# Kernel optimization log

Hardware: AMD Instinct MI355X
Metric: run time of the kernel (lower is better)

The kernel has to match this reference:

```python
import jax, jax.numpy as jnp
import numpy as np

N, E = 10000, 320000
IN_F, OUT_F = 512, 256
ALPHA = 0.2  # leaky_relu negative slope
NEG_BIG = -9e15


def setup_inputs() -> dict:
    key = jax.random.key(0)
    k1, k2, k3, k4 = jax.random.split(key, 4)
    x = jax.random.normal(k1, (N, IN_F), dtype=jnp.float32)
    # fc: Linear(in_features, out_features) -> W [out, in], b [out] (init to 0 per reset_parameters)
    W = jax.random.normal(k2, (OUT_F, IN_F), dtype=jnp.float32) * (1.414 / np.sqrt(IN_F))
    b = jnp.zeros((OUT_F,), dtype=jnp.float32)
    # att: Conv1d(1,1,2*out) == dot with vector a [2*out]
    a = jax.random.normal(k3, (2 * OUT_F,), dtype=jnp.float32) * (1.414 / np.sqrt(2 * OUT_F))
    edge_list = jax.random.randint(k4, (2, E), 0, N, dtype=jnp.int64)
    return {"x": x, "W": W, "b": b, "a": a, "edge_list": edge_list}


def reference(x, W, b, a, edge_list):
    # eval mode: dropout is identity
    src, tgt = edge_list[0], edge_list[1]
    h = x @ W.T + b  # [N, out]
    out_f = h.shape[1]
    # conv1d over concatenated [h_src, h_tgt] with kernel length 2*out == split dot product
    score = h[src] @ a[:out_f] + h[tgt] @ a[out_f:]  # [E]
    score = jax.nn.leaky_relu(score, negative_slope=ALPHA)
    n = x.shape[0]
    # torch.sparse.FloatTensor(...).to_dense() sums duplicate edges -> scatter-add
    adj = jnp.zeros((n, n), dtype=h.dtype).at[src, tgt].add(score)
    adj = jnp.where(adj == 0, jnp.asarray(NEG_BIG, h.dtype), adj)
    adj = jax.nn.softmax(adj, axis=1)
    return adj @ h  # [N, out]
```

## Files before the change

kernel.cpp:

```cpp
#include <hip/hip_runtime.h>
#include <hip/hip_bf16.h>
#include <math.h>

#define IN_F 512
#define OUT_F 256
#define ALPHA 0.2f
#define CAP 512
#define NCHAIN 16

typedef __attribute__((ext_vector_type(8))) short bf16x8;
typedef __attribute__((ext_vector_type(4))) float f32x4;

static __device__ __forceinline__ unsigned short f2bf(float f) {
  unsigned int u = __builtin_bit_cast(unsigned int, f);
  unsigned int r = (u + 0x7FFFu + ((u >> 16) & 1u)) >> 16;
  return (unsigned short)r;
}

__global__ __launch_bounds__(256) void mega(const float* __restrict__ x,
                                            const float* __restrict__ W,
                                            const float* __restrict__ bias,
                                            const float* __restrict__ a,
                                            const int* __restrict__ edges,
                                            unsigned short* __restrict__ hb,
                                            float* __restrict__ s1p,
                                            float* __restrict__ s2p,
                                            float* __restrict__ hsump,
                                            int* __restrict__ head,
                                            int2* __restrict__ rec,
                                            int N_, int E_, int mtiles, int gblocks) {
  const int tid = threadIdx.x;
  const int vb = blockIdx.x;

  if (vb >= gblocks) {
    int idx = (vb - gblocks) * 256 + tid;
    if (idx < E_) {
      int srcv = edges[idx];
      int tgtv = edges[E_ + idx];
      int old = atomicExch(&head[srcv * NCHAIN + (idx & (NCHAIN - 1))], idx);
      rec[idx] = make_int2(old, tgtv);
    }
    return;
  }

  __shared__ unsigned short lA[64][72];
  __shared__ unsigned short lB[64][72];
  __shared__ float s1t[64], s2t[64], ht[64];

  const int bm = (vb % mtiles) * 64;
  const int bn4 = vb / mtiles;
  const int bn = bn4 * 64;
  const int wave = tid >> 6, lane = tid & 63;
  const int wr = wave >> 1, wc = wave & 1;
  const int lr = lane & 15, lk = lane >> 4;

  f32x4 acc[2][2] = {};

  for (int k0 = 0; k0 < IN_F; k0 += 64) {
#pragma unroll
    for (int r = 0; r < 4; ++r) {
      int idx = tid + r * 256;
      int row = idx >> 4, c4 = idx & 15;
      int gm = bm + row;
      float4 va = (gm < N_) ? *(const float4*)&x[(size_t)gm * IN_F + k0 + c4 * 4]
                            : make_float4(0.f, 0.f, 0.f, 0.f);
      ushort4 oa;
      oa.x = f2bf(va.x); oa.y = f2bf(va.y); oa.z = f2bf(va.z); oa.w = f2bf(va.w);
      *(ushort4*)&lA[row][c4 * 4] = oa;
      float4 vbq = *(const float4*)&W[(size_t)(bn + row) * IN_F + k0 + c4 * 4];
      ushort4 ob;
      ob.x = f2bf(vbq.x); ob.y = f2bf(vbq.y); ob.z = f2bf(vbq.z); ob.w = f2bf(vbq.w);
      *(ushort4*)&lB[row][c4 * 4] = ob;
    }
    __syncthreads();
#pragma unroll
    for (int kk = 0; kk < 64; kk += 32) {
      bf16x8 af[2], bfr[2];
#pragma unroll
      for (int fm = 0; fm < 2; ++fm)
        af[fm] = *(const bf16x8*)&lA[wr * 32 + fm * 16 + lr][kk + lk * 8];
#pragma unroll
      for (int fn = 0; fn < 2; ++fn)
        bfr[fn] = *(const bf16x8*)&lB[wc * 32 + fn * 16 + lr][kk + lk * 8];
#pragma unroll
      for (int fm = 0; fm < 2; ++fm)
#pragma unroll
        for (int fn = 0; fn < 2; ++fn)
          acc[fm][fn] = __builtin_amdgcn_mfma_f32_16x16x32_bf16(af[fm], bfr[fn],
                                                                acc[fm][fn], 0, 0, 0);
    }
    __syncthreads();
  }

  if (tid < 64) { s1t[tid] = 0.f; s2t[tid] = 0.f; ht[tid] = 0.f; }
  __syncthreads();

  int gc[2];
  float av[2], bv[2], biasv[2], csum[2] = {0.f, 0.f};
#pragma unroll
  for (int fn = 0; fn < 2; ++fn) {
    gc[fn] = bn + wc * 32 + fn * 16 + lr;
    av[fn] = a[gc[fn]];
    bv[fn] = a[OUT_F + gc[fn]];
    biasv[fn] = bias[gc[fn]];
  }
#pragma unroll
  for (int fm = 0; fm < 2; ++fm) {
#pragma unroll
    for (int i = 0; i < 4; ++i) {
      int lrow = wr * 32 + fm * 16 + lk * 4 + i;
      int gr = bm + lrow;
      bool valid = (gr < N_);
      float v0 = valid ? acc[fm][0][i] + biasv[0] : 0.f;
      float v1 = valid ? acc[fm][1][i] + biasv[1] : 0.f;
      if (valid) {
        hb[(size_t)gr * OUT_F + gc[0]] = f2bf(v0);
        hb[(size_t)gr * OUT_F + gc[1]] = f2bf(v1);
      }
      csum[0] += v0; csum[1] += v1;
      float p1 = v0 * av[0] + v1 * av[1];
      float p2 = v0 * bv[0] + v1 * bv[1];
#pragma unroll
      for (int off = 1; off < 16; off <<= 1) {
        p1 += __shfl_xor(p1, off);
        p2 += __shfl_xor(p2, off);
      }
      if (lr == 0) {
        atomicAdd(&s1t[lrow], p1);
        atomicAdd(&s2t[lrow], p2);
      }
    }
  }
#pragma unroll
  for (int off = 16; off < 64; off <<= 1) {
    csum[0] += __shfl_xor(csum[0], off);
    csum[1] += __shfl_xor(csum[1], off);
  }
  if (lk == 0) {
    atomicAdd(&ht[wc * 32 + 0 * 16 + lr], csum[0]);
    atomicAdd(&ht[wc * 32 + 1 * 16 + lr], csum[1]);
  }
  __syncthreads();

  if (tid < 64) {
    int gr = bm + tid;
    if (gr < N_) {
      s1p[(size_t)gr * 4 + bn4] = s1t[tid];
      s2p[(size_t)gr * 4 + bn4] = s2t[tid];
    }
    hsump[(size_t)(bm >> 6) * OUT_F + bn + tid] = ht[tid];
  }
}

__global__ __launch_bounds__(256) void rowk(const unsigned short* __restrict__ hb,
                                            const float* __restrict__ s1p,
                                            const float* __restrict__ s2p,
                                            const float* __restrict__ hsump,
                                            int* __restrict__ head,
                                            const int2* __restrict__ rec,
                                            float* __restrict__ out,
                                            int N_, int E_, int mtiles) {
  __shared__ int s_tgt[2][CAP];
  __shared__ float s_w[2][CAP];
  __shared__ int s_len[2][NCHAIN];
  __shared__ int s_base[2][NCHAIN + 1];
  __shared__ float s_red[2][4];

  const int tid = threadIdx.x;
  const float invN = 1.0f / (float)N_;
  const int half = tid >> 7;
  const int t = tid & 127;
  const int lane = t & 63, wv = t >> 6;

  int row = blockIdx.x * 2 + half;
  bool rv = (row < N_);

  if (t < NCHAIN) {
    int len = 0;
    if (rv) {
      int e = head[row * NCHAIN + t];
      while (e >= 0 && e < E_ && len < CAP) { ++len; e = rec[e].x; }
    }
    s_len[half][t] = len;
  }
  __syncthreads();
  if (t == 0) {
    int run = 0;
#pragma unroll
    for (int c = 0; c < NCHAIN; ++c) { s_base[half][c] = run; run += s_len[half][c]; }
    s_base[half][NCHAIN] = run;
  }
  __syncthreads();
  int deg = s_base[half][NCHAIN];
  if (deg > CAP) deg = CAP;

  if (rv && t < NCHAIN) {
    int e = head[row * NCHAIN + t];
    int i = s_base[half][t];
    int cnt = 0;
    while (e >= 0 && e < E_ && cnt < CAP) {
      int2 rr = rec[e];
      if (i < CAP) s_tgt[half][i] = rr.y;
      ++i; ++cnt;
      e = rr.x;
    }
    head[row * NCHAIN + t] = -1;
  }
  __syncthreads();

  float s1i = 0.f;
  if (rv) {
    float4 sv = *(const float4*)&s1p[(size_t)row * 4];
    s1i = (sv.x + sv.y) + (sv.z + sv.w);
  }
  for (int q = t; q < deg; q += 128) {
    int tg = s_tgt[half][q];
    float4 s2v = *(const float4*)&s2p[(size_t)tg * 4];
    float s = s1i + ((s2v.x + s2v.y) + (s2v.z + s2v.w));
    s_w[half][q] = (s > 0.f) ? s : ALPHA * s;
  }
  __syncthreads();

  for (int q = t; q < deg; q += 128) {
    int tg = s_tgt[half][q];
    int first = q, cnt = 0;
    for (int j = 0; j < deg; ++j) {
      int tj = s_tgt[half][j];
      cnt += (tj == tg);
      if (tj == tg && j < first) first = j;
    }
    float v;
    if (first == q) {
      v = (float)cnt * s_w[half][q];
      if (v == 0.f) v = -INFINITY;
    } else {
      v = -INFINITY;
    }
    s_w[half][q] = v;
  }

  float m = -INFINITY;
  for (int q = t; q < deg; q += 128) m = fmaxf(m, s_w[half][q]);
#pragma unroll
  for (int off = 32; off; off >>= 1) m = fmaxf(m, __shfl_xor(m, off));
  if (lane == 0) s_red[half][wv] = m;
  __syncthreads();
  m = fmaxf(s_red[half][0], s_red[half][1]);

  bool uniform = (deg == 0) || (m == -INFINITY);

  float dsum = 0.f;
  if (!uniform) {
    for (int q = t; q < deg; q += 128) {
      float e = __expf(s_w[half][q] - m);
      s_w[half][q] = e;
      dsum += e;
    }
  }
#pragma unroll
  for (int off = 32; off; off >>= 1) dsum += __shfl_xor(dsum, off);
  if (lane == 0) s_red[half][2 + wv] = dsum;
  __syncthreads();
  float inv = 1.0f / (s_red[half][2] + s_red[half][3]);

  if (rv) {
    float2* out2 = (float2*)(out + (size_t)row * OUT_F);
    if (uniform) {
      float A = 0.f, B = 0.f;
      for (int mt = 0; mt < mtiles; ++mt) {
        A += hsump[(size_t)mt * OUT_F + 2 * t];
        B += hsump[(size_t)mt * OUT_F + 2 * t + 1];
      }
      out2[t] = make_float2(A * invN, B * invN);
    } else {
      const unsigned int* hu = (const unsigned int*)hb;
      float L0 = 0.f, L1 = 0.f, L2 = 0.f, L3 = 0.f, L4 = 0.f, L5 = 0.f, L6 = 0.f, L7 = 0.f;
      float H0 = 0.f, H1 = 0.f, H2 = 0.f, H3 = 0.f, H4 = 0.f, H5 = 0.f, H6 = 0.f, H7 = 0.f;
      int q = 0;
      for (; q + 8 <= deg; q += 8) {
        int t0 = s_tgt[half][q],     t1 = s_tgt[half][q + 1];
        int t2 = s_tgt[half][q + 2], t3 = s_tgt[half][q + 3];
        int t4 = s_tgt[half][q + 4], t5 = s_tgt[half][q + 5];
        int t6 = s_tgt[half][q + 6], t7 = s_tgt[half][q + 7];
        float w0 = s_w[half][q],     w1 = s_w[half][q + 1];
        float w2 = s_w[half][q + 2], w3 = s_w[half][q + 3];
        float w4 = s_w[half][q + 4], w5 = s_w[half][q + 5];
        float w6 = s_w[half][q + 6], w7 = s_w[half][q + 7];
        unsigned int u0 = hu[(size_t)t0 * 128 + t], u1 = hu[(size_t)t1 * 128 + t];
        unsigned int u2 = hu[(size_t)t2 * 128 + t], u3 = hu[(size_t)t3 * 128 + t];
        unsigned int u4 = hu[(size_t)t4 * 128 + t], u5 = hu[(size_t)t5 * 128 + t];
        unsigned int u6 = hu[(size_t)t6 * 128 + t], u7 = hu[(size_t)t7 * 128 + t];
        L0 += w0 * __builtin_bit_cast(float, u0 << 16);
        H0 += w0 * __builtin_bit_cast(float, u0 & 0xffff0000u);
        L1 += w1 * __builtin_bit_cast(float, u1 << 16);
        H1 += w1 * __builtin_bit_cast(float, u1 & 0xffff0000u);
        L2 += w2 * __builtin_bit_cast(float, u2 << 16);
        H2 += w2 * __builtin_bit_cast(float, u2 & 0xffff0000u);
        L3 += w3 * __builtin_bit_cast(float, u3 << 16);
        H3 += w3 * __builtin_bit_cast(float, u3 & 0xffff0000u);
        L4 += w4 * __builtin_bit_cast(float, u4 << 16);
        H4 += w4 * __builtin_bit_cast(float, u4 & 0xffff0000u);
        L5 += w5 * __builtin_bit_cast(float, u5 << 16);
        H5 += w5 * __builtin_bit_cast(float, u5 & 0xffff0000u);
        L6 += w6 * __builtin_bit_cast(float, u6 << 16);
        H6 += w6 * __builtin_bit_cast(float, u6 & 0xffff0000u);
        L7 += w7 * __builtin_bit_cast(float, u7 << 16);
        H7 += w7 * __builtin_bit_cast(float, u7 & 0xffff0000u);
      }
      for (; q < deg; ++q) {
        float w = s_w[half][q];
        unsigned int u = hu[(size_t)s_tgt[half][q] * 128 + t];
        L0 += w * __builtin_bit_cast(float, u << 16);
        H0 += w * __builtin_bit_cast(float, u & 0xffff0000u);
      }
      float accL = ((L0 + L1) + (L2 + L3)) + ((L4 + L5) + (L6 + L7));
      float accH = ((H0 + H1) + (H2 + H3)) + ((H4 + H5) + (H6 + H7));
      out2[t] = make_float2(accL * inv, accH * inv);
    }
  }
}

extern "C" void kernel_launch(void* const* d_in, const int* in_sizes, int n_in,
                              void* d_out, int out_size, void* d_ws, size_t ws_size,
                              hipStream_t stream) {
  const float* x = (const float*)d_in[0];
  const float* W = (const float*)d_in[1];
  const float* b = (const float*)d_in[2];
  const float* a = (const float*)d_in[3];
  const int* edges = (const int*)d_in[4];
  float* out = (float*)d_out;

  int N_ = in_sizes[0] / IN_F;
  int E_ = in_sizes[4] / 2;

  char* ws = (char*)d_ws;
  size_t off = 0;
  auto alloc = [&](size_t bytes) {
    char* q = ws + off;
    off = (off + bytes + 255) & ~(size_t)255;
    return q;
  };
  int mtiles = (N_ + 63) / 64;
  unsigned short* hb    = (unsigned short*)alloc((size_t)N_ * OUT_F * sizeof(unsigned short));
  float*          s1p   = (float*)alloc((size_t)N_ * 4 * sizeof(float));
  float*          s2p   = (float*)alloc((size_t)N_ * 4 * sizeof(float));
  float*          hsump = (float*)alloc((size_t)mtiles * OUT_F * sizeof(float));
  int*            head  = (int*)alloc((size_t)NCHAIN * N_ * sizeof(int));
  int2*           rec   = (int2*)alloc((size_t)E_ * sizeof(int2));

  int gblocks = mtiles * (OUT_F / 64);
  int fblocks = (E_ + 255) / 256;

  mega<<<gblocks + fblocks, 256, 0, stream>>>(x, W, b, a, edges, hb, s1p, s2p, hsump,
                                              head, rec, N_, E_, mtiles, gblocks);
  rowk<<<(N_ + 1) / 2, 256, 0, stream>>>(hb, s1p, s2p, hsump, head, rec, out, N_, E_, mtiles);
}
```

Before: 75.08 us.

## Widen GEMM tile to full output width so attention scores need no partial sums

Each GEMM block now computes a 64-row by full 256-column tile, with each wave owning 64 columns, instead of 64x64 tiles split across four column blocks. This lets s1/s2 and column sums be reduced entirely within one block, so the per-row partial arrays (4 floats each) and their later summation in the row kernel become single scalar reads. The cost is four times fewer GEMM blocks (about 157), larger LDS use for the whole W slice, and more accumulator registers per thread. That may hurt occupancy and load balance on a GPU with many CUs.

```diff
diff --git a/kernel.cpp b/kernel.cpp
--- a/kernel.cpp
+++ b/kernel.cpp
@@ -23,17 +23,17 @@
                                             const float* __restrict__ a,
                                             const int* __restrict__ edges,
                                             unsigned short* __restrict__ hb,
-                                            float* __restrict__ s1p,
-                                            float* __restrict__ s2p,
+                                            float* __restrict__ s1,
+                                            float* __restrict__ s2,
                                             float* __restrict__ hsump,
                                             int* __restrict__ head,
                                             int2* __restrict__ rec,
-                                            int N_, int E_, int mtiles, int gblocks) {
+                                            int N_, int E_, int mtiles) {
   const int tid = threadIdx.x;
   const int vb = blockIdx.x;
 
-  if (vb >= gblocks) {
-    int idx = (vb - gblocks) * 256 + tid;
+  if (vb >= mtiles) {
+    int idx = (vb - mtiles) * 256 + tid;
     if (idx < E_) {
       int srcv = edges[idx];
       int tgtv = edges[E_ + idx];
@@ -44,17 +44,14 @@
   }
 
   __shared__ unsigned short lA[64][72];
-  __shared__ unsigned short lB[64][72];
-  __shared__ float s1t[64], s2t[64], ht[64];
-
-  const int bm = (vb % mtiles) * 64;
-  const int bn4 = vb / mtiles;
-  const int bn = bn4 * 64;
+  __shared__ unsigned short lB[256][72];
+  __shared__ float s1t[64], s2t[64], ht[OUT_F];
+
+  const int bm = vb * 64;
   const int wave = tid >> 6, lane = tid & 63;
-  const int wr = wave >> 1, wc = wave & 1;
   const int lr = lane & 15, lk = lane >> 4;
 
-  f32x4 acc[2][2] = {};
+  f32x4 acc[4][4] = {};
 
   for (int k0 = 0; k0 < IN_F; k0 += 64) {
 #pragma unroll
@@ -67,65 +64,70 @@
       ushort4 oa;
       oa.x = f2bf(va.x); oa.y = f2bf(va.y); oa.z = f2bf(va.z); oa.w = f2bf(va.w);
       *(ushort4*)&lA[row][c4 * 4] = oa;
-      float4 vbq = *(const float4*)&W[(size_t)(bn + row) * IN_F + k0 + c4 * 4];
+    }
+#pragma unroll
+    for (int r = 0; r < 16; ++r) {
+      int idx = tid + r * 256;
+      int row = idx >> 4, c4 = idx & 15;
+      float4 vb4 = *(const float4*)&W[(size_t)row * IN_F + k0 + c4 * 4];
       ushort4 ob;
-      ob.x = f2bf(vbq.x); ob.y = f2bf(vbq.y); ob.z = f2bf(vbq.z); ob.w = f2bf(vbq.w);
+      ob.x = f2bf(vb4.x); ob.y = f2bf(vb4.y); ob.z = f2bf(vb4.z); ob.w = f2bf(vb4.w);
       *(ushort4*)&lB[row][c4 * 4] = ob;
     }
     __syncthreads();
 #pragma unroll
     for (int kk = 0; kk < 64; kk += 32) {
-      bf16x8 af[2], bfr[2];
-#pragma unroll
-      for (int fm = 0; fm < 2; ++fm)
-        af[fm] = *(const bf16x8*)&lA[wr * 32 + fm * 16 + lr][kk + lk * 8];
-#pragma unroll
-      for (int fn = 0; fn < 2; ++fn)
-        bfr[fn] = *(const bf16x8*)&lB[wc * 32 + fn * 16 + lr][kk + lk * 8];
-#pragma unroll
-      for (int fm = 0; fm < 2; ++fm)
-#pragma unroll
-        for (int fn = 0; fn < 2; ++fn)
+      bf16x8 af[4], bfr[4];
+#pragma unroll
+      for (int fm = 0; fm < 4; ++fm)
+        af[fm] = *(const bf16x8*)&lA[fm * 16 + lr][kk + lk * 8];
+#pragma unroll
+      for (int fn = 0; fn < 4; ++fn)
+        bfr[fn] = *(const bf16x8*)&lB[wave * 64 + fn * 16 + lr][kk + lk * 8];
+#pragma unroll
+      for (int fm = 0; fm < 4; ++fm)
+#pragma unroll
+        for (int fn = 0; fn < 4; ++fn)
           acc[fm][fn] = __builtin_amdgcn_mfma_f32_16x16x32_bf16(af[fm], bfr[fn],
                                                                 acc[fm][fn], 0, 0, 0);
     }
     __syncthreads();
   }
 
-  if (tid < 64) { s1t[tid] = 0.f; s2t[tid] = 0.f; ht[tid] = 0.f; }
-  __syncthreads();
-
-  int gc[2];
-  float av[2], bv[2], biasv[2], csum[2] = {0.f, 0.f};
-#pragma unroll
-  for (int fn = 0; fn < 2; ++fn) {
-    gc[fn] = bn + wc * 32 + fn * 16 + lr;
-    av[fn] = a[gc[fn]];
-    bv[fn] = a[OUT_F + gc[fn]];
-    biasv[fn] = bias[gc[fn]];
-  }
-#pragma unroll
-  for (int fm = 0; fm < 2; ++fm) {
+  if (tid < 64) { s1t[tid] = 0.f; s2t[tid] = 0.f; }
+  __syncthreads();
+
+  int gcv[4];
+  float av[4], bv[4], biasv[4], csum[4] = {0.f, 0.f, 0.f, 0.f};
+#pragma unroll
+  for (int fn = 0; fn < 4; ++fn) {
+    gcv[fn] = wave * 64 + fn * 16 + lr;
+    av[fn] = a[gcv[fn]];
+    bv[fn] = a[OUT_F + gcv[fn]];
+    biasv[fn] = bias[gcv[fn]];
+  }
+#pragma unroll
+  for (int fm = 0; fm < 4; ++fm) {
 #pragma unroll
     for (int i = 0; i < 4; ++i) {
-      int lrow = wr * 32 + fm * 16 + lk * 4 + i;
+      int lrow = fm * 16 + lk * 4 + i;
       int gr = bm + lrow;
       bool valid = (gr < N_);
-      float v0 = valid ? acc[fm][0][i] + biasv[0] : 0.f;
-      float v1 = valid ? acc[fm][1][i] + biasv[1] : 0.f;
-      if (valid) {
-        hb[(size_t)gr * OUT_F + gc[0]] = f2bf(v0);
-        hb[(size_t)gr * OUT_F + gc[1]] = f2bf(v1);
-      }
-      csum[0] += v0; csum[1] += v1;
-      float p1 = v0 * av[0] + v1 * av[1];
-      float p2 = v0 * bv[0] + v1 * bv[1];
+      float v[4];
+#pragma unroll
+      for (int fn = 0; fn < 4; ++fn) {
+        v[fn] = valid ? acc[fm][fn][i] + biasv[fn] : 0.f;
+        if (valid) hb[(size_t)gr * OUT_F + gcv[fn]] = f2bf(v[fn]);
+        csum[fn] += v[fn];
+      }
+      float p1 = (v[0] * av[0] + v[1] * av[1]) + (v[2] * av[2] + v[3] * av[3]);
+      float p2 = (v[0] * bv[0] + v[1] * bv[1]) + (v[2] * bv[2] + v[3] * bv[3]);
 #pragma unroll
       for (int off = 1; off < 16; off <<= 1) {
         p1 += __shfl_xor(p1, off);
         p2 += __shfl_xor(p2, off);
       }
-      if (lr == 0) {
+      if (lr == 0 && valid) {
         atomicAdd(&s1t[lrow], p1);
         atomicAdd(&s2t[lrow], p2);
       }
@@ -133,28 +135,25 @@
   }
 #pragma unroll
   for (int off = 16; off < 64; off <<= 1) {
-    csum[0] += __shfl_xor(csum[0], off);
-    csum[1] += __shfl_xor(csum[1], off);
+#pragma unroll
+    for (int fn = 0; fn < 4; ++fn) csum[fn] += __shfl_xor(csum[fn], off);
   }
   if (lk == 0) {
-    atomicAdd(&ht[wc * 32 + 0 * 16 + lr], csum[0]);
-    atomicAdd(&ht[wc * 32 + 1 * 16 + lr], csum[1]);
+#pragma unroll
+    for (int fn = 0; fn < 4; ++fn) ht[gcv[fn]] = csum[fn];
   }
   __syncthreads();
 
   if (tid < 64) {
     int gr = bm + tid;
-    if (gr < N_) {
-      s1p[(size_t)gr * 4 + bn4] = s1t[tid];
-      s2p[(size_t)gr * 4 + bn4] = s2t[tid];
-    }
-    hsump[(size_t)(bm >> 6) * OUT_F + bn + tid] = ht[tid];
-  }
+    if (gr < N_) { s1[gr] = s1t[tid]; s2[gr] = s2t[tid]; }
+  }
+  hsump[(size_t)vb * OUT_F + tid] = ht[tid];
 }
 
 __global__ __launch_bounds__(256) void rowk(const unsigned short* __restrict__ hb,
-                                            const float* __restrict__ s1p,
-                                            const float* __restrict__ s2p,
+                                            const float* __restrict__ s1,
+                                            const float* __restrict__ s2,
                                             const float* __restrict__ hsump,
                                             int* __restrict__ head,
                                             const int2* __restrict__ rec,
@@ -208,15 +207,10 @@
   }
   __syncthreads();
 
-  float s1i = 0.f;
-  if (rv) {
-    float4 sv = *(const float4*)&s1p[(size_t)row * 4];
-    s1i = (sv.x + sv.y) + (sv.z + sv.w);
-  }
+  float s1i = rv ? s1[row] : 0.f;
   for (int q = t; q < deg; q += 128) {
     int tg = s_tgt[half][q];
-    float4 s2v = *(const float4*)&s2p[(size_t)tg * 4];
-    float s = s1i + ((s2v.x + s2v.y) + (s2v.z + s2v.w));
+    float s = s1i + s2[tg];
     s_w[half][q] = (s > 0.f) ? s : ALPHA * s;
   }
   __syncthreads();
@@ -342,16 +336,15 @@
   };
   int mtiles = (N_ + 63) / 64;
   unsigned short* hb    = (unsigned short*)alloc((size_t)N_ * OUT_F * sizeof(unsigned short));
-  float*          s1p   = (float*)alloc((size_t)N_ * 4 * sizeof(float));
-  float*          s2p   = (float*)alloc((size_t)N_ * 4 * sizeof(float));
+  float*          s1    = (float*)alloc((size_t)N_ * sizeof(float));
+  float*          s2    = (float*)alloc((size_t)N_ * sizeof(float));
   float*          hsump = (float*)alloc((size_t)mtiles * OUT_F * sizeof(float));
   int*            head  = (int*)alloc((size_t)NCHAIN * N_ * sizeof(int));
   int2*           rec   = (int2*)alloc((size_t)E_ * sizeof(int2));
 
-  int gblocks = mtiles * (OUT_F / 64);
   int fblocks = (E_ + 255) / 256;
 
-  mega<<<gblocks + fblocks, 256, 0, stream>>>(x, W, b, a, edges, hb, s1p, s2p, hsump,
-                                              head, rec, N_, E_, mtiles, gblocks);
-  rowk<<<(N_ + 1) / 2, 256, 0, stream>>>(hb, s1p, s2p, hsump, head, rec, out, N_, E_, mtiles);
+  mega<<<mtiles + fblocks, 256, 0, stream>>>(x, W, b, a, edges, hb, s1, s2, hsump,
+                                             head, rec, N_, E_, mtiles);
+  rowk<<<(N_ + 1) / 2, 256, 0, stream>>>(hb, s1, s2, hsump, head, rec, out, N_, E_, mtiles);
 }
```

After: 78.87 us. 5.0% more time.

## Use 32-row GEMM tiles and one row per block with atomic-slot chain gather

Applied to the files above, without the earlier changes.

The projection GEMM now uses 32x64 tiles, with each wave owning a 16-column strip, so twice as many blocks are launched to spread work across more CUs. The row kernel now processes one row per 128-thread block instead of two rows per 256-thread block. Its two-pass chain walk (count lengths, prefix sum, then fill) is replaced by a single pass that claims slots through a shared atomic counter. This drops one traversal of the linked lists and removes the cross-half coupling. In exchange, x is re-read less efficiently per W tile, W is reloaded by twice as many blocks, and neighbour order becomes nondeterministic, which can change the floating-point summation order.

```diff
diff --git a/kernel.cpp b/kernel.cpp
--- a/kernel.cpp
+++ b/kernel.cpp
@@ -28,7 +28,7 @@
                                             float* __restrict__ hsump,
                                             int* __restrict__ head,
                                             int2* __restrict__ rec,
-                                            int N_, int E_, int mtiles, int gblocks) {
+                                            int N_, int E_, int m32, int gblocks) {
   const int tid = threadIdx.x;
   const int vb = blockIdx.x;
 
@@ -43,22 +43,22 @@
     return;
   }
 
-  __shared__ unsigned short lA[64][72];
+  __shared__ unsigned short lA[32][72];
   __shared__ unsigned short lB[64][72];
-  __shared__ float s1t[64], s2t[64], ht[64];
-
-  const int bm = (vb % mtiles) * 64;
-  const int bn4 = vb / mtiles;
+  __shared__ float s1t[32], s2t[32], ht[64];
+
+  const int mt = vb % m32;
+  const int bn4 = vb / m32;
+  const int bm = mt * 32;
   const int bn = bn4 * 64;
   const int wave = tid >> 6, lane = tid & 63;
-  const int wr = wave >> 1, wc = wave & 1;
   const int lr = lane & 15, lk = lane >> 4;
 
-  f32x4 acc[2][2] = {};
+  f32x4 acc[2] = {};
 
   for (int k0 = 0; k0 < IN_F; k0 += 64) {
 #pragma unroll
-    for (int r = 0; r < 4; ++r) {
+    for (int r = 0; r < 2; ++r) {
       int idx = tid + r * 256;
       int row = idx >> 4, c4 = idx & 15;
       int gm = bm + row;
@@ -67,256 +67,212 @@
       ushort4 oa;
       oa.x = f2bf(va.x); oa.y = f2bf(va.y); oa.z = f2bf(va.z); oa.w = f2bf(va.w);
       *(ushort4*)&lA[row][c4 * 4] = oa;
-      float4 vbq = *(const float4*)&W[(size_t)(bn + row) * IN_F + k0 + c4 * 4];
+    }
+#pragma unroll
+    for (int r = 0; r < 4; ++r) {
+      int idx = tid + r * 256;
+      int row = idx >> 4, c4 = idx & 15;
+      float4 vb4 = *(const float4*)&W[(size_t)(bn + row) * IN_F + k0 + c4 * 4];
       ushort4 ob;
-      ob.x = f2bf(vbq.x); ob.y = f2bf(vbq.y); ob.z = f2bf(vbq.z); ob.w = f2bf(vbq.w);
+      ob.x = f2bf(vb4.x); ob.y = f2bf(vb4.y); ob.z = f2bf(vb4.z); ob.w = f2bf(vb4.w);
       *(ushort4*)&lB[row][c4 * 4] = ob;
     }
     __syncthreads();
 #pragma unroll
     for (int kk = 0; kk < 64; kk += 32) {
-      bf16x8 af[2], bfr[2];
+      bf16x8 af[2], bfr;
 #pragma unroll
       for (int fm = 0; fm < 2; ++fm)
-        af[fm] = *(const bf16x8*)&lA[wr * 32 + fm * 16 + lr][kk + lk * 8];
-#pragma unroll
-      for (int fn = 0; fn < 2; ++fn)
-        bfr[fn] = *(const bf16x8*)&lB[wc * 32 + fn * 16 + lr][kk + lk * 8];
+        af[fm] = *(const bf16x8*)&lA[fm * 16 + lr][kk + lk * 8];
+      bfr = *(const bf16x8*)&lB[wave * 16 + lr][kk + lk * 8];
 #pragma unroll
       for (int fm = 0; fm < 2; ++fm)
-#pragma unroll
-        for (int fn = 0; fn < 2; ++fn)
-          acc[fm][fn] = __builtin_amdgcn_mfma_f32_16x16x32_bf16(af[fm], bfr[fn],
-                                                                acc[fm][fn], 0, 0, 0);
+        acc[fm] = __builtin_amdgcn_mfma_f32_16x16x32_bf16(af[fm], bfr, acc[fm], 0, 0, 0);
     }
     __syncthreads();
   }
 
-  if (tid < 64) { s1t[tid] = 0.f; s2t[tid] = 0.f; ht[tid] = 0.f; }
-  __syncthreads();
-
-  int gc[2];
-  float av[2], bv[2], biasv[2], csum[2] = {0.f, 0.f};
-#pragma unroll
-  for (int fn = 0; fn < 2; ++fn) {
-    gc[fn] = bn + wc * 32 + fn * 16 + lr;
-    av[fn] = a[gc[fn]];
-    bv[fn] = a[OUT_F + gc[fn]];
-    biasv[fn] = bias[gc[fn]];
-  }
+  if (tid < 32) { s1t[tid] = 0.f; s2t[tid] = 0.f; }
+  __syncthreads();
+
+  const int gcv = bn + wave * 16 + lr;
+  const float av = a[gcv], bv2 = a[OUT_F + gcv], biasv = bias[gcv];
+  float csum = 0.f;
 #pragma unroll
   for (int fm = 0; fm < 2; ++fm) {
 #pragma unroll
     for (int i = 0; i < 4; ++i) {
-      int lrow = wr * 32 + fm * 16 + lk * 4 + i;
+      int lrow = fm * 16 + lk * 4 + i;
       int gr = bm + lrow;
       bool valid = (gr < N_);
-      float v0 = valid ? acc[fm][0][i] + biasv[0] : 0.f;
-      float v1 = valid ? acc[fm][1][i] + biasv[1] : 0.f;
-      if (valid) {
-        hb[(size_t)gr * OUT_F + gc[0]] = f2bf(v0);
-        hb[(size_t)gr * OUT_F + gc[1]] = f2bf(v1);
-      }
-      csum[0] += v0; csum[1] += v1;
-      float p1 = v0 * av[0] + v1 * av[1];
-      float p2 = v0 * bv[0] + v1 * bv[1];
+      float v = valid ? acc[fm][i] + biasv : 0.f;
+      if (valid) hb[(size_t)gr * OUT_F + gcv] = f2bf(v);
+      csum += v;
+      float p1 = v * av;
+      float p2 = v * bv2;
 #pragma unroll
       for (int off = 1; off < 16; off <<= 1) {
         p1 += __shfl_xor(p1, off);
         p2 += __shfl_xor(p2, off);
       }
-      if (lr == 0) {
+      if (lr == 0 && valid) {
         atomicAdd(&s1t[lrow], p1);
         atomicAdd(&s2t[lrow], p2);
       }
     }
   }
 #pragma unroll
-  for (int off = 16; off < 64; off <<= 1) {
-    csum[0] += __shfl_xor(csum[0], off);
-    csum[1] += __shfl_xor(csum[1], off);
-  }
-  if (lk == 0) {
-    atomicAdd(&ht[wc * 32 + 0 * 16 + lr], csum[0]);
-    atomicAdd(&ht[wc * 32 + 1 * 16 + lr], csum[1]);
-  }
-  __syncthreads();
-
-  if (tid < 64) {
+  for (int off = 16; off < 64; off <<= 1) csum += __shfl_xor(csum, off);
+  if (lk == 0) ht[wave * 16 + lr] = csum;
+  __syncthreads();
+
+  if (tid < 32) {
     int gr = bm + tid;
     if (gr < N_) {
       s1p[(size_t)gr * 4 + bn4] = s1t[tid];
       s2p[(size_t)gr * 4 + bn4] = s2t[tid];
     }
-    hsump[(size_t)(bm >> 6) * OUT_F + bn + tid] = ht[tid];
-  }
+  }
+  if (tid < 64) hsump[(size_t)mt * OUT_F + bn + tid] = ht[tid];
 }
 
-__global__ __launch_bounds__(256) void rowk(const unsigned short* __restrict__ hb,
+__global__ __launch_bounds__(128) void rowk(const unsigned short* __restrict__ hb,
                                             const float* __restrict__ s1p,
                                             const float* __restrict__ s2p,
                                             const float* __restrict__ hsump,
                                             int* __restrict__ head,
                                             const int2* __restrict__ rec,
                                             float* __restrict__ out,
-                                            int N_, int E_, int mtiles) {
-  __shared__ int s_tgt[2][CAP];
-  __shared__ float s_w[2][CAP];
-  __shared__ int s_len[2][NCHAIN];
-  __shared__ int s_base[2][NCHAIN + 1];
-  __shared__ float s_red[2][4];
-
-  const int tid = threadIdx.x;
+                                            int N_, int E_, int m32) {
+  __shared__ int s_tgt[CAP];
+  __shared__ float s_w[CAP];
+  __shared__ float s_red[4];
+  __shared__ int s_cnt;
+
+  const int t = threadIdx.x;
+  const int lane = t & 63, wv = t >> 6;
+  const int row = blockIdx.x;
   const float invN = 1.0f / (float)N_;
-  const int half = tid >> 7;
-  const int t = tid & 127;
-  const int lane = t & 63, wv = t >> 6;
-
-  int row = blockIdx.x * 2 + half;
-  bool rv = (row < N_);
+
+  if (t == 0) s_cnt = 0;
+  __syncthreads();
 
   if (t < NCHAIN) {
-    int len = 0;
-    if (rv) {
-      int e = head[row * NCHAIN + t];
-      while (e >= 0 && e < E_ && len < CAP) { ++len; e = rec[e].x; }
-    }
-    s_len[half][t] = len;
-  }
-  __syncthreads();
-  if (t == 0) {
-    int run = 0;
-#pragma unroll
-    for (int c = 0; c < NCHAIN; ++c) { s_base[half][c] = run; run += s_len[half][c]; }
-    s_base[half][NCHAIN] = run;
-  }
-  __syncthreads();
-  int deg = s_base[half][NCHAIN];
+    int e = head[row * NCHAIN + t];
+    int guard = 0;
+    while (e >= 0 && e < E_ && guard < CAP) {
+      int2 rr = rec[e];
+      int slot = atomicAdd(&s_cnt, 1);
+      if (slot < CAP) s_tgt[slot] = rr.y;
+      ++guard;
+      e = rr.x;
+    }
+    head[row * NCHAIN + t] = -1;
+  }
+  __syncthreads();
+  int deg = s_cnt;
   if (deg > CAP) deg = CAP;
 
-  if (rv && t < NCHAIN) {
-    int e = head[row * NCHAIN + t];
-    int i = s_base[half][t];
-    int cnt = 0;
-    while (e >= 0 && e < E_ && cnt < CAP) {
-      int2 rr = rec[e];
-      if (i < CAP) s_tgt[half][i] = rr.y;
-      ++i; ++cnt;
-      e = rr.x;
-    }
-    head[row * NCHAIN + t] = -1;
-  }
-  __syncthreads();
-
-  float s1i = 0.f;
-  if (rv) {
-    float4 sv = *(const float4*)&s1p[(size_t)row * 4];
-    s1i = (sv.x + sv.y) + (sv.z + sv.w);
-  }
+  float4 sv = *(const float4*)&s1p[(size_t)row * 4];
+  float s1i = (sv.x + sv.y) + (sv.z + sv.w);
   for (int q = t; q < deg; q += 128) {
-    int tg = s_tgt[half][q];
+    int tg = s_tgt[q];
     float4 s2v = *(const float4*)&s2p[(size_t)tg * 4];
     float s = s1i + ((s2v.x + s2v.y) + (s2v.z + s2v.w));
-    s_w[half][q] = (s > 0.f) ? s : ALPHA * s;
+    s_w[q] = (s > 0.f) ? s : ALPHA * s;
   }
   __syncthreads();
 
   for (int q = t; q < deg; q += 128) {
-    int tg = s_tgt[half][q];
+    int tg = s_tgt[q];
     int first = q, cnt = 0;
     for (int j = 0; j < deg; ++j) {
-      int tj = s_tgt[half][j];
+      int tj = s_tgt[j];
       cnt += (tj == tg);
       if (tj == tg && j < first) first = j;
     }
     float v;
     if (first == q) {
-      v = (float)cnt * s_w[half][q];
+      v = (float)cnt * s_w[q];
       if (v == 0.f) v = -INFINITY;
     } else {
       v = -INFINITY;
     }
-    s_w[half][q] = v;
+    s_w[q] = v;
   }
 
   float m = -INFINITY;
-  for (int q = t; q < deg; q += 128) m = fmaxf(m, s_w[half][q]);
+  for (int q = t; q < deg; q += 128) m = fmaxf(m, s_w[q]);
 #pragma unroll
   for (int off = 32; off; off >>= 1) m = fmaxf(m, __shfl_xor(m, off));
-  if (lane == 0) s_red[half][wv] = m;
-  __syncthreads();
-  m = fmaxf(s_red[half][0], s_red[half][1]);
+  if (lane == 0) s_red[wv] = m;
+  __syncthreads();
+  m = fmaxf(s_red[0], s_red[1]);
 
   bool uniform = (deg == 0) || (m == -INFINITY);
 
   float dsum = 0.f;
   if (!uniform) {
     for (int q = t; q < deg; q += 128) {
-      float e = __expf(s_w[half][q] - m);
-      s_w[half][q] = e;
+      float e = __expf(s_w[q] - m);
+      s_w[q] = e;
       dsum += e;
     }
   }
 #pragma unroll
   for (int off = 32; off; off >>= 1) dsum += __shfl_xor(dsum, off);
-  if (lane == 0) s_red[half][2 + wv] = dsum;
-  __syncthreads();
-  float inv = 1.0f / (s_red[half][2] + s_red[half][3]);
-
-  if (rv) {
-    float2* out2 = (float2*)(out + (size_t)row * OUT_F);
-    if (uniform) {
-      float A = 0.f, B = 0.f;
-      for (int mt = 0; mt < mtiles; ++mt) {
-        A += hsump[(size_t)mt * OUT_F + 2 * t];
-        B += hsump[(size_t)mt * OUT_F + 2 * t + 1];
-      }
-      out2[t] = make_float2(A * invN, B * invN);
-    } else {
-      const unsigned int* hu = (const unsigned int*)hb;
-      float L0 = 0.f, L1 = 0.f, L2 = 0.f, L3 = 0.f, L4 = 0.f, L5 = 0.f, L6 = 0.f, L7 = 0.f;
-      float H0 = 0.f, H1 = 0.f, H2 = 0.f, H3 = 0.f, H4 = 0.f, H5 = 0.f, H6 = 0.f, H7 = 0.f;
-      int q = 0;
-      for (; q + 8 <= deg; q += 8) {
-        int t0 = s_tgt[half][q],     t1 = s_tgt[half][q + 1];
-        int t2 = s_tgt[half][q + 2], t3 = s_tgt[half][q + 3];
-        int t4 = s_tgt[half][q + 4], t5 = s_tgt[half][q + 5];
-        int t6 = s_tgt[half][q + 6], t7 = s_tgt[half][q + 7];
-        float w0 = s_w[half][q],     w1 = s_w[half][q + 1];
-        float w2 = s_w[half][q + 2], w3 = s_w[half][q + 3];
-        float w4 = s_w[half][q + 4], w5 = s_w[half][q + 5];
-        float w6 = s_w[half][q + 6], w7 = s_w[half][q + 7];
-        unsigned int u0 = hu[(size_t)t0 * 128 + t], u1 = hu[(size_t)t1 * 128 + t];
-        unsigned int u2 = hu[(size_t)t2 * 128 + t], u3 = hu[(size_t)t3 * 128 + t];
-        unsigned int u4 = hu[(size_t)t4 * 128 + t], u5 = hu[(size_t)t5 * 128 + t];
-        unsigned int u6 = hu[(size_t)t6 * 128 + t], u7 = hu[(size_t)t7 * 128 + t];
-        L0 += w0 * __builtin_bit_cast(float, u0 << 16);
-        H0 += w0 * __builtin_bit_cast(float, u0 & 0xffff0000u);
-        L1 += w1 * __builtin_bit_cast(float, u1 << 16);
-        H1 += w1 * __builtin_bit_cast(float, u1 & 0xffff0000u);
-        L2 += w2 * __builtin_bit_cast(float, u2 << 16);
-        H2 += w2 * __builtin_bit_cast(float, u2 & 0xffff0000u);
-        L3 += w3 * __builtin_bit_cast(float, u3 << 16);
-        H3 += w3 * __builtin_bit_cast(float, u3 & 0xffff0000u);
-        L4 += w4 * __builtin_bit_cast(float, u4 << 16);
-        H4 += w4 * __builtin_bit_cast(float, u4 & 0xffff0000u);
-        L5 += w5 * __builtin_bit_cast(float, u5 << 16);
-        H5 += w5 * __builtin_bit_cast(float, u5 & 0xffff0000u);
-        L6 += w6 * __builtin_bit_cast(float, u6 << 16);
-        H6 += w6 * __builtin_bit_cast(float, u6 & 0xffff0000u);
-        L7 += w7 * __builtin_bit_cast(float, u7 << 16);
-        H7 += w7 * __builtin_bit_cast(float, u7 & 0xffff0000u);
-      }
-      for (; q < deg; ++q) {
-        float w = s_w[half][q];
-        unsigned int u = hu[(size_t)s_tgt[half][q] * 128 + t];
-        L0 += w * __builtin_bit_cast(float, u << 16);
-        H0 += w * __builtin_bit_cast(float, u & 0xffff0000u);
-      }
-      float accL = ((L0 + L1) + (L2 + L3)) + ((L4 + L5) + (L6 + L7));
-      float accH = ((H0 + H1) + (H2 + H3)) + ((H4 + H5) + (H6 + H7));
-      out2[t] = make_float2(accL * inv, accH * inv);
-    }
+  if (lane == 0) s_red[2 + wv] = dsum;
+  __syncthreads();
+  float inv = 1.0f / (s_red[2] + s_red[3]);
+
+  float2* out2 = (float2*)(out + (size_t)row * OUT_F);
+  if (uniform) {
+    float A = 0.f, B = 0.f;
+    for (int mt = 0; mt < m32; ++mt) {
+      A += hsump[(size_t)mt * OUT_F + 2 * t];
+      B += hsump[(size_t)mt * OUT_F + 2 * t + 1];
+    }
+    out2[t] = make_float2(A * invN, B * invN);
+  } else {
+    const unsigned int* hu = (const unsigned int*)hb;
+    float L0 = 0.f, L1 = 0.f, L2 = 0.f, L3 = 0.f, L4 = 0.f, L5 = 0.f, L6 = 0.f, L7 = 0.f;
+    float H0 = 0.f, H1 = 0.f, H2 = 0.f, H3 = 0.f, H4 = 0.f, H5 = 0.f, H6 = 0.f, H7 = 0.f;
+    int q = 0;
+    for (; q + 8 <= deg; q += 8) {
+      int t0 = s_tgt[q],     t1 = s_tgt[q + 1], t2 = s_tgt[q + 2], t3 = s_tgt[q + 3];
+      int t4 = s_tgt[q + 4], t5 = s_tgt[q + 5], t6 = s_tgt[q + 6], t7 = s_tgt[q + 7];
+      float w0 = s_w[q],     w1 = s_w[q + 1], w2 = s_w[q + 2], w3 = s_w[q + 3];
+      float w4 = s_w[q + 4], w5 = s_w[q + 5], w6 = s_w[q + 6], w7 = s_w[q + 7];
+      unsigned int u0 = hu[(size_t)t0 * 128 + t], u1 = hu[(size_t)t1 * 128 + t];
+      unsigned int u2 = hu[(size_t)t2 * 128 + t], u3 = hu[(size_t)t3 * 128 + t];
+      unsigned int u4 = hu[(size_t)t4 * 128 + t], u5 = hu[(size_t)t5 * 128 + t];
+      unsigned int u6 = hu[(size_t)t6 * 128 + t], u7 = hu[(size_t)t7 * 128 + t];
+      L0 += w0 * __builtin_bit_cast(float, u0 << 16);
+      H0 += w0 * __builtin_bit_cast(float, u0 & 0xffff0000u);
+      L1 += w1 * __builtin_bit_cast(float, u1 << 16);
+      H1 += w1 * __builtin_bit_cast(float, u1 & 0xffff0000u);
+      L2 += w2 * __builtin_bit_cast(float, u2 << 16);
+      H2 += w2 * __builtin_bit_cast(float, u2 & 0xffff0000u);
+      L3 += w3 * __builtin_bit_cast(float, u3 << 16);
+      H3 += w3 * __builtin_bit_cast(float, u3 & 0xffff0000u);
+      L4 += w4 * __builtin_bit_cast(float, u4 << 16);
+      H4 += w4 * __builtin_bit_cast(float, u4 & 0xffff0000u);
+      L5 += w5 * __builtin_bit_cast(float, u5 << 16);
+      H5 += w5 * __builtin_bit_cast(float, u5 & 0xffff0000u);
+      L6 += w6 * __builtin_bit_cast(float, u6 << 16);
+      H6 += w6 * __builtin_bit_cast(float, u6 & 0xffff0000u);
+      L7 += w7 * __builtin_bit_cast(float, u7 << 16);
+      H7 += w7 * __builtin_bit_cast(float, u7 & 0xffff0000u);
+    }
+    for (; q < deg; ++q) {
+      float w = s_w[q];
+      unsigned int u = hu[(size_t)s_tgt[q] * 128 + t];
+      L0 += w * __builtin_bit_cast(float, u << 16);
+      H0 += w * __builtin_bit_cast(float, u & 0xffff0000u);
+    }
+    float accL = ((L0 + L1) + (L2 + L3)) + ((L4 + L5) + (L6 + L7));
+    float accH = ((H0 + H1) + (H2 + H3)) + ((H4 + H5) + (H6 + H7));
+    out2[t] = make_float2(accL * inv, accH * inv);
   }
 }
 
@@ -340,18 +296,18 @@
     off = (off + bytes + 255) & ~(size_t)255;
     return q;
   };
-  int mtiles = (N_ + 63) / 64;
+  int m32 = (N_ + 31) / 32;
   unsigned short* hb    = (unsigned short*)alloc((size_t)N_ * OUT_F * sizeof(unsigned short));
   float*          s1p   = (float*)alloc((size_t)N_ * 4 * sizeof(float));
   float*          s2p   = (float*)alloc((size_t)N_ * 4 * sizeof(float));
-  float*          hsump = (float*)alloc((size_t)mtiles * OUT_F * sizeof(float));
+  float*          hsump = (float*)alloc((size_t)m32 * OUT_F * sizeof(float));
   int*            head  = (int*)alloc((size_t)NCHAIN * N_ * sizeof(int));
   int2*           rec   = (int2*)alloc((size_t)E_ * sizeof(int2));
 
-  int gblocks = mtiles * (OUT_F / 64);
+  int gblocks = m32 * 4;
   int fblocks = (E_ + 255) / 256;
 
   mega<<<gblocks + fblocks, 256, 0, stream>>>(x, W, b, a, edges, hb, s1p, s2p, hsump,
-                                              head, rec, N_, E_, mtiles, gblocks);
-  rowk<<<(N_ + 1) / 2, 256, 0, stream>>>(hb, s1p, s2p, hsump, head, rec, out, N_, E_, mtiles);
+                                              head, rec, N_, E_, m32, gblocks);
+  rowk<<<N_, 128, 0, stream>>>(hb, s1p, s2p, hsump, head, rec, out, N_, E_, m32);
 }
```

Measured after the change: 64.78 us. 1.16x faster.
